# Kernel tuning notes

Hardware: AMD Instinct MI355X
Metric: run time of the kernel (lower is better)

Reference implementation:

```python
import jax, jax.numpy as jnp
import numpy as np

K = 9      # kernel_size
H = 6      # num_head
HD = 64    # head_dim
D = H * HD # reduced_hidden_dim = 384
B, S = 16, 1024
OUT = 384  # hidden_dim // 2


def setup_inputs() -> dict:
    key = jax.random.key(0)
    k = jax.random.split(key, 5)
    q = jax.random.normal(k[0], (B, S, D), dtype=jnp.float32)
    ks = jax.random.normal(k[1], (B, S, D), dtype=jnp.float32)
    v = jax.random.normal(k[2], (B, S, D), dtype=jnp.float32)
    Wk = jax.random.normal(k[3], (K * H, D), dtype=jnp.float32) * 0.02
    bk = jnp.zeros((K * H,), dtype=jnp.float32)
    Wp = jax.random.normal(k[4], (OUT, D), dtype=jnp.float32) * 0.02
    bp = jnp.zeros((OUT,), dtype=jnp.float32)
    return {"q": q, "ks": ks, "v": v, "Wk": Wk, "bk": bk, "Wp": Wp, "bp": bp}


def reference(q, ks, v, Wk, bk, Wp, bp):
    b, s, d = v.shape
    pad = K // 2
    # expand4conv: zero-pad along seq and gather K-wide sliding windows
    vp = jnp.pad(v, ((0, 0), (pad, pad), (0, 0)))            # [B, S+K-1, D]
    win = jnp.stack([vp[:, i:i + s] for i in range(K)], -1)  # [B, S, D, K]
    win = win.reshape(b, s, H, HD, K)                        # [B, S, H, HD, K]
    # dynamic kernel: softmax over kernel taps
    logits = jnp.einsum('bsd,od->bso', q * ks, Wk) + bk       # [B, S, K*H]
    dk = jax.nn.softmax(logits.reshape(b, s, H, K), axis=-1)  # [B, S, H, K]
    # local weighted reduction over the window
    out = jnp.einsum('bshdk,bshk->bshd', win, dk).reshape(b, s, d)
    return jnp.einsum('bsd,od->bso', out, Wp) + bp            # [B, S, OUT]
```

## Files before the change

kernel.cpp:

```cpp
#include <hip/hip_runtime.h>
#include <hip/hip_bf16.h>

#define BB 16
#define SS 1024
#define DD 384
#define HH 6
#define KK 9
#define KH 54
#define OUTD 384
#define NKT 12
#define VLD 392

typedef __attribute__((ext_vector_type(4))) float floatx4;
typedef __attribute__((ext_vector_type(8))) __bf16 bf16x8;
typedef __attribute__((ext_vector_type(4))) __bf16 bf16x4;

__global__ __launch_bounds__(256) void cast_kernel(const float* __restrict__ Wk,
                                                   const float* __restrict__ Wp,
                                                   __bf16* __restrict__ WkT,
                                                   __bf16* __restrict__ WpT) {
    int i = blockIdx.x * 256 + threadIdx.x;
    if (i < 4 * NKT * 64 * 8) {
        int e = i & 7, lane = (i >> 3) & 63, t = i >> 9;
        int kstep = t % NKT, ntile = t / NKT;
        int row = ntile * 16 + (lane & 15);
        int col = kstep * 32 + ((lane >> 4) << 3) + e;
        WkT[i] = (row < KH) ? (__bf16)Wk[row * DD + col] : (__bf16)0.0f;
    } else if (i < 24576 + 24 * NKT * 64 * 8) {
        int j = i - 24576;
        int e = j & 7, lane = (j >> 3) & 63, t = j >> 9;
        int kstep = t % NKT, ntile = t / NKT;
        int row = ntile * 16 + (lane & 15);
        int col = kstep * 32 + ((lane >> 4) << 3) + e;
        WpT[j] = (__bf16)Wp[row * DD + col];
    }
}

__global__ __launch_bounds__(256, 4) void fused_kernel(const float* __restrict__ q,
                                                       const float* __restrict__ ks,
                                                       const float* __restrict__ v,
                                                       const __bf16* __restrict__ WkT,
                                                       const float* __restrict__ bk,
                                                       const __bf16* __restrict__ WpT,
                                                       const float* __restrict__ bp,
                                                       float* __restrict__ out) {
    __shared__ __bf16 vqS[24 * VLD];
    __shared__ float  dkS[16 * 56];
    __shared__ __align__(16) char uS[16 * VLD * 2];
    float*  lgS = (float*)uS;
    __bf16* aS  = (__bf16*)uS;

    const int tid  = threadIdx.x;
    const int wave = tid >> 6;
    const int lane = tid & 63;
    const int m0   = blockIdx.x * 16;
    const int b    = blockIdx.x >> 6;
    const int s0   = (blockIdx.x & 63) * 16;
    const int fr   = lane & 15;
    const int fk   = (lane >> 4) * 8;
    const int col_in = lane & 15;
    const int rgrp   = (lane >> 4) * 4;

    {
        const float* qb = q  + (size_t)m0 * DD;
        const float* kb = ks + (size_t)m0 * DD;
#pragma unroll
        for (int it = 0; it < 6; ++it) {
            int c = tid + it * 256;
            int row = c / 96, col = (c % 96) * 4;
            floatx4 qv = *reinterpret_cast<const floatx4*>(qb + (size_t)row * DD + col);
            floatx4 kv = *reinterpret_cast<const floatx4*>(kb + (size_t)row * DD + col);
            floatx4 pr = qv * kv;
            bf16x4 pk = { (__bf16)pr.x, (__bf16)pr.y, (__bf16)pr.z, (__bf16)pr.w };
            *reinterpret_cast<bf16x4*>(&vqS[row * VLD + col]) = pk;
        }
    }
    __syncthreads();

    {
        floatx4 acc = {};
#pragma unroll
        for (int s = 0; s < NKT; ++s) {
            bf16x8 af = *reinterpret_cast<const bf16x8*>(&vqS[fr * VLD + s * 32 + fk]);
            bf16x8 bf = *reinterpret_cast<const bf16x8*>(
                WkT + (((wave * NKT + s) * 64 + lane) << 3));
            acc = __builtin_amdgcn_mfma_f32_16x16x32_bf16(af, bf, acc, 0, 0, 0);
        }
#pragma unroll
        for (int r = 0; r < 4; ++r)
            lgS[(rgrp + r) * 66 + wave * 16 + col_in] = acc[r];
    }
    __syncthreads();

    if (tid < 16 * HH) {
        int row = tid / HH, h = tid % HH;
        float lg[KK];
        float mx = -1e30f;
#pragma unroll
        for (int k = 0; k < KK; ++k) {
            float s = lgS[row * 66 + h * KK + k] + bk[h * KK + k];
            lg[k] = s;
            mx = fmaxf(mx, s);
        }
        float sum = 0.0f;
#pragma unroll
        for (int k = 0; k < KK; ++k) { lg[k] = __expf(lg[k] - mx); sum += lg[k]; }
        float inv = 1.0f / sum;
#pragma unroll
        for (int k = 0; k < KK; ++k) dkS[row * 56 + h * KK + k] = lg[k] * inv;
    }

    {
        const float* vb = v + (size_t)b * SS * DD;
        if (s0 != 0 && s0 != SS - 16) {
#pragma unroll
            for (int it = 0; it < 9; ++it) {
                int c = tid + it * 256;
                int row = c / 96, col = (c % 96) * 4;
                floatx4 val = *reinterpret_cast<const floatx4*>(
                    vb + (size_t)(s0 + row - 4) * DD + col);
                bf16x4 vk = { (__bf16)val.x, (__bf16)val.y, (__bf16)val.z, (__bf16)val.w };
                *reinterpret_cast<bf16x4*>(&vqS[row * VLD + col]) = vk;
            }
        } else {
#pragma unroll
            for (int it = 0; it < 9; ++it) {
                int c = tid + it * 256;
                int row = c / 96, col = (c % 96) * 4;
                int r = s0 + row - 4;
                floatx4 val = {};
                if (r >= 0 && r < SS)
                    val = *reinterpret_cast<const floatx4*>(vb + (size_t)r * DD + col);
                bf16x4 vk = { (__bf16)val.x, (__bf16)val.y, (__bf16)val.z, (__bf16)val.w };
                *reinterpret_cast<bf16x4*>(&vqS[row * VLD + col]) = vk;
            }
        }
    }
    __syncthreads();

#pragma unroll
    for (int it = 0; it < 6; ++it) {
        int p = tid + it * 256;
        int row = p / 96, c4 = p % 96;
        int h = c4 >> 4;
        const float* dkr = &dkS[row * 56 + h * KK];
        floatx4 a = {};
#pragma unroll
        for (int k = 0; k < KK; ++k) {
            bf16x4 w = *reinterpret_cast<const bf16x4*>(&vqS[(row + k) * VLD + c4 * 4]);
            floatx4 wf = { (float)w[0], (float)w[1], (float)w[2], (float)w[3] };
            a += wf * dkr[k];
        }
        bf16x4 o = { (__bf16)a.x, (__bf16)a.y, (__bf16)a.z, (__bf16)a.w };
        *reinterpret_cast<bf16x4*>(&aS[row * VLD + c4 * 4]) = o;
    }
    __syncthreads();

    {
        const int nt0 = wave * 6;
        floatx4 acc[6] = {};
#pragma unroll
        for (int s = 0; s < NKT; ++s) {
            bf16x8 af = *reinterpret_cast<const bf16x8*>(&aS[fr * VLD + s * 32 + fk]);
#pragma unroll
            for (int j = 0; j < 6; ++j) {
                bf16x8 bf = *reinterpret_cast<const bf16x8*>(
                    WpT + ((((nt0 + j) * NKT + s) * 64 + lane) << 3));
                acc[j] = __builtin_amdgcn_mfma_f32_16x16x32_bf16(af, bf, acc[j], 0, 0, 0);
            }
        }
        float* ob = out + (size_t)m0 * OUTD;
#pragma unroll
        for (int j = 0; j < 6; ++j) {
            int col = (nt0 + j) * 16 + col_in;
            float bv = bp[col];
#pragma unroll
            for (int r = 0; r < 4; ++r)
                ob[(size_t)(rgrp + r) * OUTD + col] = acc[j][r] + bv;
        }
    }
}

extern "C" void kernel_launch(void* const* d_in, const int* in_sizes, int n_in,
                              void* d_out, int out_size, void* d_ws, size_t ws_size,
                              hipStream_t stream) {
    const float* q  = (const float*)d_in[0];
    const float* ks = (const float*)d_in[1];
    const float* v  = (const float*)d_in[2];
    const float* Wk = (const float*)d_in[3];
    const float* bk = (const float*)d_in[4];
    const float* Wp = (const float*)d_in[5];
    const float* bp = (const float*)d_in[6];
    float* out = (float*)d_out;

    __bf16* WkT = (__bf16*)d_ws;
    __bf16* WpT = (__bf16*)((char*)d_ws + 49152);

    cast_kernel<<<(24576 + 147456 + 255) / 256, 256, 0, stream>>>(Wk, Wp, WkT, WpT);
    fused_kernel<<<(BB * SS) / 16, 256, 0, stream>>>(q, ks, v, WkT, bk, WpT, bp, out);
}
```

Measured before the change: 124.6 us.

## Double rows per block to 32 with 512 threads and prefetch v early

Each block now handles 32 sequence rows with 8 waves instead of 16 rows with 4 waves. This halves the redundant halo loads of v and the per-block reloads of the Wk/Wp weight fragments, since each B fragment in the output GEMM now feeds two row tiles. The v window is loaded into registers before the logits GEMM so its global latency overlaps the MFMA and softmax work. In exchange the block uses more LDS and registers (8 float4 prefetch regs), which may cut occupancy, and the block count halves to 512.

Result: no change. 124.9 us (+0.2%).

```diff
diff --git a/kernel.cpp b/kernel.cpp
--- a/kernel.cpp
+++ b/kernel.cpp
@@ -10,6 +10,8 @@
 #define OUTD 384
 #define NKT 12
 #define VLD 392
+#define RPB 32
+#define NTH 512
 
 typedef __attribute__((ext_vector_type(4))) float floatx4;
 typedef __attribute__((ext_vector_type(8))) __bf16 bf16x8;
@@ -36,7 +38,7 @@
     }
 }
 
-__global__ __launch_bounds__(256, 4) void fused_kernel(const float* __restrict__ q,
+__global__ __launch_bounds__(NTH, 4) void fused_kernel(const float* __restrict__ q,
                                                        const float* __restrict__ ks,
                                                        const float* __restrict__ v,
                                                        const __bf16* __restrict__ WkT,
@@ -44,18 +46,18 @@
                                                        const __bf16* __restrict__ WpT,
                                                        const float* __restrict__ bp,
                                                        float* __restrict__ out) {
-    __shared__ __bf16 vqS[24 * VLD];
-    __shared__ float  dkS[16 * 56];
-    __shared__ __align__(16) char uS[16 * VLD * 2];
+    __shared__ __bf16 vqS[40 * VLD];
+    __shared__ float  dkS[RPB * 56];
+    __shared__ __align__(16) char uS[RPB * VLD * 2];
     float*  lgS = (float*)uS;
     __bf16* aS  = (__bf16*)uS;
 
     const int tid  = threadIdx.x;
     const int wave = tid >> 6;
     const int lane = tid & 63;
-    const int m0   = blockIdx.x * 16;
-    const int b    = blockIdx.x >> 6;
-    const int s0   = (blockIdx.x & 63) * 16;
+    const int m0   = blockIdx.x * RPB;
+    const int b    = blockIdx.x >> 5;
+    const int s0   = (blockIdx.x & 31) * RPB;
     const int fr   = lane & 15;
     const int fk   = (lane >> 4) * 8;
     const int col_in = lane & 15;
@@ -66,7 +68,7 @@
         const float* kb = ks + (size_t)m0 * DD;
 #pragma unroll
         for (int it = 0; it < 6; ++it) {
-            int c = tid + it * 256;
+            int c = tid + it * NTH;
             int row = c / 96, col = (c % 96) * 4;
             floatx4 qv = *reinterpret_cast<const floatx4*>(qb + (size_t)row * DD + col);
             floatx4 kv = *reinterpret_cast<const floatx4*>(kb + (size_t)row * DD + col);
@@ -75,24 +77,42 @@
             *reinterpret_cast<bf16x4*>(&vqS[row * VLD + col]) = pk;
         }
     }
-    __syncthreads();
-
-    {
+
+    floatx4 vpre[8];
+    {
+        const float* vb = v + (size_t)b * SS * DD;
+#pragma unroll
+        for (int it = 0; it < 8; ++it) {
+            int c = tid + it * NTH;
+            int row = c / 96, col = (c % 96) * 4;
+            int r = s0 + row - 4;
+            int rc = r < 0 ? 0 : (r > SS - 1 ? SS - 1 : r);
+            floatx4 val = *reinterpret_cast<const floatx4*>(vb + (size_t)rc * DD + col);
+            if (r < 0 || r >= SS) val = floatx4{0.0f, 0.0f, 0.0f, 0.0f};
+            vpre[it] = val;
+        }
+    }
+    __syncthreads();
+
+    {
+        const int rt = wave >> 2;
+        const int nt = wave & 3;
         floatx4 acc = {};
 #pragma unroll
         for (int s = 0; s < NKT; ++s) {
-            bf16x8 af = *reinterpret_cast<const bf16x8*>(&vqS[fr * VLD + s * 32 + fk]);
-            bf16x8 bf = *reinterpret_cast<const bf16x8*>(
-                WkT + (((wave * NKT + s) * 64 + lane) << 3));
-            acc = __builtin_amdgcn_mfma_f32_16x16x32_bf16(af, bf, acc, 0, 0, 0);
+            bf16x8 af = *reinterpret_cast<const bf16x8*>(
+                &vqS[(rt * 16 + fr) * VLD + s * 32 + fk]);
+            bf16x8 bfrag = *reinterpret_cast<const bf16x8*>(
+                WkT + (((nt * NKT + s) * 64 + lane) << 3));
+            acc = __builtin_amdgcn_mfma_f32_16x16x32_bf16(af, bfrag, acc, 0, 0, 0);
         }
 #pragma unroll
         for (int r = 0; r < 4; ++r)
-            lgS[(rgrp + r) * 66 + wave * 16 + col_in] = acc[r];
-    }
-    __syncthreads();
-
-    if (tid < 16 * HH) {
+            lgS[(rt * 16 + rgrp + r) * 66 + nt * 16 + col_in] = acc[r];
+    }
+    __syncthreads();
+
+    if (tid < RPB * HH) {
         int row = tid / HH, h = tid % HH;
         float lg[KK];
         float mx = -1e30f;
@@ -111,36 +131,22 @@
     }
 
     {
-        const float* vb = v + (size_t)b * SS * DD;
-        if (s0 != 0 && s0 != SS - 16) {
-#pragma unroll
-            for (int it = 0; it < 9; ++it) {
-                int c = tid + it * 256;
+#pragma unroll
+        for (int it = 0; it < 8; ++it) {
+            int c = tid + it * NTH;
+            if (c < 3840) {
                 int row = c / 96, col = (c % 96) * 4;
-                floatx4 val = *reinterpret_cast<const floatx4*>(
-                    vb + (size_t)(s0 + row - 4) * DD + col);
+                floatx4 val = vpre[it];
                 bf16x4 vk = { (__bf16)val.x, (__bf16)val.y, (__bf16)val.z, (__bf16)val.w };
                 *reinterpret_cast<bf16x4*>(&vqS[row * VLD + col]) = vk;
             }
-        } else {
-#pragma unroll
-            for (int it = 0; it < 9; ++it) {
-                int c = tid + it * 256;
-                int row = c / 96, col = (c % 96) * 4;
-                int r = s0 + row - 4;
-                floatx4 val = {};
-                if (r >= 0 && r < SS)
-                    val = *reinterpret_cast<const floatx4*>(vb + (size_t)r * DD + col);
-                bf16x4 vk = { (__bf16)val.x, (__bf16)val.y, (__bf16)val.z, (__bf16)val.w };
-                *reinterpret_cast<bf16x4*>(&vqS[row * VLD + col]) = vk;
-            }
         }
     }
     __syncthreads();
 
 #pragma unroll
     for (int it = 0; it < 6; ++it) {
-        int p = tid + it * 256;
+        int p = tid + it * NTH;
         int row = p / 96, c4 = p % 96;
         int h = c4 >> 4;
         const float* dkr = &dkS[row * 56 + h * KK];
@@ -157,26 +163,30 @@
     __syncthreads();
 
     {
-        const int nt0 = wave * 6;
-        floatx4 acc[6] = {};
+        const int nt0 = wave * 3;
+        floatx4 acc[2][3] = {};
 #pragma unroll
         for (int s = 0; s < NKT; ++s) {
-            bf16x8 af = *reinterpret_cast<const bf16x8*>(&aS[fr * VLD + s * 32 + fk]);
-#pragma unroll
-            for (int j = 0; j < 6; ++j) {
-                bf16x8 bf = *reinterpret_cast<const bf16x8*>(
+            bf16x8 a0 = *reinterpret_cast<const bf16x8*>(&aS[fr * VLD + s * 32 + fk]);
+            bf16x8 a1 = *reinterpret_cast<const bf16x8*>(&aS[(16 + fr) * VLD + s * 32 + fk]);
+#pragma unroll
+            for (int j = 0; j < 3; ++j) {
+                bf16x8 bfrag = *reinterpret_cast<const bf16x8*>(
                     WpT + ((((nt0 + j) * NKT + s) * 64 + lane) << 3));
-                acc[j] = __builtin_amdgcn_mfma_f32_16x16x32_bf16(af, bf, acc[j], 0, 0, 0);
+                acc[0][j] = __builtin_amdgcn_mfma_f32_16x16x32_bf16(a0, bfrag, acc[0][j], 0, 0, 0);
+                acc[1][j] = __builtin_amdgcn_mfma_f32_16x16x32_bf16(a1, bfrag, acc[1][j], 0, 0, 0);
             }
         }
         float* ob = out + (size_t)m0 * OUTD;
 #pragma unroll
-        for (int j = 0; j < 6; ++j) {
+        for (int j = 0; j < 3; ++j) {
             int col = (nt0 + j) * 16 + col_in;
             float bv = bp[col];
 #pragma unroll
-            for (int r = 0; r < 4; ++r)
-                ob[(size_t)(rgrp + r) * OUTD + col] = acc[j][r] + bv;
+            for (int rt = 0; rt < 2; ++rt)
+#pragma unroll
+                for (int r = 0; r < 4; ++r)
+                    ob[(size_t)(rt * 16 + rgrp + r) * OUTD + col] = acc[rt][j][r] + bv;
         }
     }
 }
@@ -197,5 +207,5 @@
     __bf16* WpT = (__bf16*)((char*)d_ws + 49152);
 
     cast_kernel<<<(24576 + 147456 + 255) / 256, 256, 0, stream>>>(Wk, Wp, WkT, WpT);
-    fused_kernel<<<(BB * SS) / 16, 256, 0, stream>>>(q, ks, v, WkT, bk, WpT, bp, out);
+    fused_kernel<<<(BB * SS) / RPB, NTH, 0, stream>>>(q, ks, v, WkT, bk, WpT, bp, out);
 }
```
